# Kernel optimization log

Hardware: AMD Instinct MI355X
Metric: run time of the kernel (lower is better)

Reference implementation:

```python
import jax, jax.numpy as jnp
import numpy as np

NUM_USERS = 100_000
NUM_ITEMS = 400_000
N = NUM_USERS + NUM_ITEMS  # total nodes in bipartite graph
EMB = 64
N_LAYERS = 3
NNZ = 10_000_000


def setup_inputs() -> dict:
    key = jax.random.key(0)
    k1, k2, k3, k4, k5 = jax.random.split(key, 5)
    user_embeddings = jax.random.normal(k1, (NUM_USERS, EMB), dtype=jnp.float32)
    item_embeddings = jax.random.normal(k2, (NUM_ITEMS, EMB), dtype=jnp.float32)
    adj_rows = jax.random.randint(k3, (NNZ,), 0, N, dtype=jnp.int32)
    adj_cols = jax.random.randint(k4, (NNZ,), 0, N, dtype=jnp.int32)
    # symmetric-normalized adjacency values are small positive floats
    adj_vals = jax.random.uniform(k5, (NNZ,), dtype=jnp.float32) * 0.1
    return {
        "user_embeddings": user_embeddings,
        "item_embeddings": item_embeddings,
        "adj_vals": adj_vals,
        "adj_rows": adj_rows,
        "adj_cols": adj_cols,
    }


def _spmm(vals, rows, cols, x):
    # out[r] = sum_{nz : rows[nz]==r} vals[nz] * x[cols[nz]]
    return jax.ops.segment_sum(vals[:, None] * x[cols], rows, num_segments=N)


def reference(user_embeddings, item_embeddings, adj_vals, adj_rows, adj_cols):
    ego = jnp.concatenate([user_embeddings, item_embeddings], axis=0)  # [N, EMB]
    acc = ego
    for _ in range(N_LAYERS):
        ego = _spmm(adj_vals, adj_rows, adj_cols, ego)
        acc = acc + ego
    all_emb = acc / jnp.asarray(N_LAYERS + 1, dtype=ego.dtype)  # layer-mean
    return all_emb[:NUM_USERS], all_emb[NUM_USERS:]
```

## Files before the change

kernel.cpp:

```cpp
#include <hip/hip_runtime.h>


#define NUSERS 100000
#define NNODES 500000
#define EMB 64
#define COLBITS 19
#define CMASK ((1u << COLBITS) - 1u)

#define SBBITS 10
#define SBROWS (1 << SBBITS)
#define SBMASK (SBROWS - 1)
#define NSB ((NNODES + SBROWS - 1) / SBROWS)
#define TILE 7168
#define P2_THREADS 1024
#define P2_K 24
#define P2_CAP (P2_THREADS * P2_K)
#define SLACK_PAIRS 262144

typedef unsigned long long ull;

__device__ __forceinline__ unsigned pk2(float lo, float hi) {
  unsigned a = __float_as_uint(lo);
  unsigned b = __float_as_uint(hi);
  a = (a + 0x7fffu + ((a >> 16) & 1u)) >> 16;
  b = (b + 0x7fffu + ((b >> 16) & 1u)) & 0xffff0000u;
  return (a & 0xffffu) | b;
}
__device__ __forceinline__ float blo(unsigned u) { return __uint_as_float(u << 16); }
__device__ __forceinline__ float bhi(unsigned u) { return __uint_as_float(u & 0xffff0000u); }


__global__ void hist_sb(const int* __restrict__ rows, int nnz,
                        int* __restrict__ counts) {
  __shared__ int h[NSB];
  for (int i = threadIdx.x; i < NSB; i += blockDim.x) h[i] = 0;
  __syncthreads();
  int i = blockIdx.x * blockDim.x + threadIdx.x;
  int stride = gridDim.x * blockDim.x;
  for (; i < nnz; i += stride) atomicAdd(&h[rows[i] >> SBBITS], 1);
  __syncthreads();
  for (int j = threadIdx.x; j < NSB; j += blockDim.x)
    if (h[j]) atomicAdd(&counts[j], h[j]);
}

__global__ void scan_buckets(const int* __restrict__ counts,
                             int* __restrict__ bptr, int* __restrict__ cursor,
                             int n, int nnz) {
  __shared__ int s[512];
  const int t = threadIdx.x;
  const int base = t * 8;
  int e[8];
  int tsum = 0;
#pragma unroll
  for (int j = 0; j < 8; ++j) {
    e[j] = (base + j < n) ? counts[base + j] : 0;
    tsum += e[j];
  }
  s[t] = tsum;
  __syncthreads();
  for (int off = 1; off < 512; off <<= 1) {
    int v = (t >= off) ? s[t - off] : 0;
    __syncthreads();
    s[t] += v;
    __syncthreads();
  }
  int run = s[t] - tsum;
#pragma unroll
  for (int j = 0; j < 8; ++j) {
    if (base + j < n) { bptr[base + j] = run; cursor[base + j] = run; }
    run += e[j];
  }
  if (t == 511) bptr[n] = nnz;
}

__global__ __launch_bounds__(256) void scatter_sb(
    const int* __restrict__ rows, const int* __restrict__ cols,
    const float* __restrict__ vals, int nnz,
    int* __restrict__ cursor, ull* __restrict__ pairs) {
  __shared__ ull stg[TILE];
  __shared__ int cnt[NSB];
  __shared__ int start[NSB];
  __shared__ int sbase[NSB];
  __shared__ int ssc[256];
  const int t = threadIdx.x;
  const int tile0 = blockIdx.x * TILE;
  const int tileN = min(TILE, nnz - tile0);
  if (tileN <= 0) return;

  for (int i = t; i < NSB; i += 256) cnt[i] = 0;
  __syncthreads();

  int rr[TILE / 256];
#pragma unroll
  for (int k = 0; k < TILE / 256; ++k) {
    int idx = tile0 + t + k * 256;
    rr[k] = (idx < nnz) ? rows[idx] : -1;
    if (rr[k] >= 0) atomicAdd(&cnt[rr[k] >> SBBITS], 1);
  }
  __syncthreads();

  {
    const int i0 = 2 * t, i1 = 2 * t + 1;
    int c0 = (i0 < NSB) ? cnt[i0] : 0;
    int c1 = (i1 < NSB) ? cnt[i1] : 0;
    int tsum = c0 + c1;
    ssc[t] = tsum;
    __syncthreads();
    for (int off = 1; off < 256; off <<= 1) {
      int v = (t >= off) ? ssc[t - off] : 0;
      __syncthreads();
      ssc[t] += v;
      __syncthreads();
    }
    int excl = ssc[t] - tsum;
    if (i0 < NSB) start[i0] = excl;
    if (i1 < NSB) start[i1] = excl + c0;
  }
  __syncthreads();

  for (int sb = t; sb < NSB; sb += 256) {
    int c = cnt[sb];
    if (c) sbase[sb] = atomicAdd(&cursor[sb], c);
  }
  __syncthreads();
  for (int i = t; i < NSB; i += 256) cnt[i] = 0;
  __syncthreads();

#pragma unroll
  for (int k = 0; k < TILE / 256; ++k) {
    int idx = tile0 + t + k * 256;
    if (idx < nnz) {
      int r = rr[k];
      int sb = r >> SBBITS;
      unsigned key = ((unsigned)(r & SBMASK) << COLBITS) | (unsigned)cols[idx];
      ull p = ((ull)__float_as_uint(vals[idx]) << 32) | key;
      int j = start[sb] + atomicAdd(&cnt[sb], 1);
      stg[j] = p;
    }
  }
  __syncthreads();

  for (int j = t; j < tileN; j += 256) {
    int lo = 0, hi = NSB - 1;
    while (lo < hi) {
      int mid = (lo + hi + 1) >> 1;
      if (start[mid] <= j) lo = mid; else hi = mid - 1;
    }
    pairs[sbase[lo] + (j - start[lo])] = stg[j];
  }
}

__global__ __launch_bounds__(P2_THREADS) void finalize_sb(
    const int* __restrict__ bptr, ull* __restrict__ pairs,
    int* __restrict__ rs, int* __restrict__ re,
    int* __restrict__ ovf_alloc, int nnz) {
  __shared__ int hist[SBROWS];
  __shared__ int start[SBROWS];
  __shared__ int cur[SBROWS];
  __shared__ int ovf_base;
  const int b = blockIdx.x;
  const int t = threadIdx.x;
  const int s = bptr[b];
  const int n = bptr[b + 1] - s;
  const bool ovf = (n > P2_CAP);

  hist[t] = 0;
  ull* __restrict__ slack = pairs + nnz;
  if (ovf && t == 0) ovf_base = atomicAdd(ovf_alloc, n);
  __syncthreads();

  ull q[P2_K];
  if (!ovf) {
#pragma unroll
    for (int k = 0; k < P2_K; ++k) {
      int idx = t + k * P2_THREADS;
      if (idx < n) {
        q[k] = pairs[s + idx];
        atomicAdd(&hist[(unsigned)q[k] >> COLBITS], 1);
      }
    }
  } else {
    for (int j = t; j < n; j += P2_THREADS) slack[ovf_base + j] = pairs[s + j];
    __syncthreads();
    for (int j = t; j < n; j += P2_THREADS)
      atomicAdd(&hist[(unsigned)slack[ovf_base + j] >> COLBITS], 1);
  }
  __syncthreads();

  start[t] = hist[t];
  __syncthreads();
  for (int off = 1; off < SBROWS; off <<= 1) {
    int v = (t >= off) ? start[t - off] : 0;
    __syncthreads();
    start[t] += v;
    __syncthreads();
  }
  int excl = start[t] - hist[t];
  cur[t] = excl;

  int row = b * SBROWS + t;
  if (row < NNODES) {
    rs[row] = s + excl;
    re[row] = s + excl + hist[t];
  }
  __syncthreads();

  if (!ovf) {
#pragma unroll
    for (int k = 0; k < P2_K; ++k) {
      int idx = t + k * P2_THREADS;
      if (idx < n) {
        unsigned key = (unsigned)q[k];
        int pos = atomicAdd(&cur[key >> COLBITS], 1);
        pairs[s + pos] = ((q[k] >> 32) << 32) | (key & CMASK);
      }
    }
  } else {
    for (int j = t; j < n; j += P2_THREADS) {
      ull p = slack[ovf_base + j];
      unsigned key = (unsigned)p;
      int pos = atomicAdd(&cur[key >> COLBITS], 1);
      pairs[s + pos] = ((p >> 32) << 32) | (key & CMASK);
    }
  }
}

__global__ void conv_e16(const float4* __restrict__ user4,
                         const float4* __restrict__ item4,
                         uint2* __restrict__ E) {
  const int n4 = NNODES * EMB / 4;
  const int u4 = NUSERS * EMB / 4;
  int i = blockIdx.x * blockDim.x + threadIdx.x;
  if (i >= n4) return;
  float4 a = (i < u4) ? user4[i] : item4[i - u4];
  E[i] = make_uint2(pk2(a.x, a.y), pk2(a.z, a.w));
}

template <bool FINAL>
__global__ __launch_bounds__(256) void spmm_bf16(
    const int* __restrict__ rs, const int* __restrict__ re,
    const ull* __restrict__ pq, const ushort* __restrict__ T,
    const float* __restrict__ user_emb, const float* __restrict__ item_emb,
    void* __restrict__ dest, float scale) {
  const int lane = threadIdx.x & 63;
  const int sub  = lane >> 3;
  const int l4   = lane & 7;
  const int wid  = (int)((blockIdx.x * blockDim.x + threadIdx.x) >> 6);
  const int r = wid * 8 + sub;
  if (r >= NNODES) return;
  const int s = rs[r];
  const int e = re[r];
  const uint4* __restrict__ T4 = (const uint4*)T;

  float4 aL0 = make_float4(0.f, 0.f, 0.f, 0.f);
  float4 aH0 = make_float4(0.f, 0.f, 0.f, 0.f);
  float4 aL1 = make_float4(0.f, 0.f, 0.f, 0.f);
  float4 aH1 = make_float4(0.f, 0.f, 0.f, 0.f);

  auto fma8 = [&](float4& L, float4& H, float v, uint4 z) {
    L.x = fmaf(v, blo(z.x), L.x); L.y = fmaf(v, bhi(z.x), L.y);
    L.z = fmaf(v, blo(z.y), L.z); L.w = fmaf(v, bhi(z.y), L.w);
    H.x = fmaf(v, blo(z.z), H.x); H.y = fmaf(v, bhi(z.z), H.y);
    H.z = fmaf(v, blo(z.w), H.z); H.w = fmaf(v, bhi(z.w), H.w);
  };

  int i = s;
  for (; i + 3 < e; i += 4) {
    ull q0 = __builtin_nontemporal_load(&pq[i + 0]);
    ull q1 = __builtin_nontemporal_load(&pq[i + 1]);
    ull q2 = __builtin_nontemporal_load(&pq[i + 2]);
    ull q3 = __builtin_nontemporal_load(&pq[i + 3]);
    uint4 z0 = T4[(size_t)(unsigned)q0 * 8 + l4];
    uint4 z1 = T4[(size_t)(unsigned)q1 * 8 + l4];
    uint4 z2 = T4[(size_t)(unsigned)q2 * 8 + l4];
    uint4 z3 = T4[(size_t)(unsigned)q3 * 8 + l4];
    float v0 = __uint_as_float((unsigned)(q0 >> 32));
    float v1 = __uint_as_float((unsigned)(q1 >> 32));
    float v2 = __uint_as_float((unsigned)(q2 >> 32));
    float v3 = __uint_as_float((unsigned)(q3 >> 32));
    fma8(aL0, aH0, v0, z0);
    fma8(aL1, aH1, v1, z1);
    fma8(aL0, aH0, v2, z2);
    fma8(aL1, aH1, v3, z3);
  }
  for (; i < e; ++i) {
    ull q = __builtin_nontemporal_load(&pq[i]);
    uint4 z = T4[(size_t)(unsigned)q * 8 + l4];
    float v = __uint_as_float((unsigned)(q >> 32));
    fma8(aL0, aH0, v, z);
  }

  float4 aL, aH;
  aL.x = aL0.x + aL1.x; aL.y = aL0.y + aL1.y;
  aL.z = aL0.z + aL1.z; aL.w = aL0.w + aL1.w;
  aH.x = aH0.x + aH1.x; aH.y = aH0.y + aH1.y;
  aH.z = aH0.z + aH1.z; aH.w = aH0.w + aH1.w;

  const ull* e0p = (r < NUSERS)
      ? (const ull*)(user_emb + (size_t)r * EMB)
      : (const ull*)(item_emb + (size_t)(r - NUSERS) * EMB);
  ull eq0 = __builtin_nontemporal_load(&e0p[l4 * 4 + 0]);
  ull eq1 = __builtin_nontemporal_load(&e0p[l4 * 4 + 1]);
  ull eq2 = __builtin_nontemporal_load(&e0p[l4 * 4 + 2]);
  ull eq3 = __builtin_nontemporal_load(&e0p[l4 * 4 + 3]);
  float e0, e1, e2, e3, e4, e5, e6, e7;
  e0 = __uint_as_float((unsigned)eq0); e1 = __uint_as_float((unsigned)(eq0 >> 32));
  e2 = __uint_as_float((unsigned)eq1); e3 = __uint_as_float((unsigned)(eq1 >> 32));
  e4 = __uint_as_float((unsigned)eq2); e5 = __uint_as_float((unsigned)(eq2 >> 32));
  e6 = __uint_as_float((unsigned)eq3); e7 = __uint_as_float((unsigned)(eq3 >> 32));

  if (FINAL) {
    float4 oL, oH;
    oL.x = scale * (e0 + aL.x); oL.y = scale * (e1 + aL.y);
    oL.z = scale * (e2 + aL.z); oL.w = scale * (e3 + aL.w);
    oH.x = scale * (e4 + aH.x); oH.y = scale * (e5 + aH.y);
    oH.z = scale * (e6 + aH.z); oH.w = scale * (e7 + aH.w);
    float4* d4 = (float4*)dest;
    d4[(size_t)r * 16 + l4 * 2 + 0] = oL;
    d4[(size_t)r * 16 + l4 * 2 + 1] = oH;
  } else {
    uint4 ob;
    ob.x = pk2(e0 + aL.x, e1 + aL.y);
    ob.y = pk2(e2 + aL.z, e3 + aL.w);
    ob.z = pk2(e4 + aH.x, e5 + aH.y);
    ob.w = pk2(e6 + aH.z, e7 + aH.w);
    ((uint4*)dest)[(size_t)r * 8 + l4] = ob;
  }
}


__global__ void spmm_atomic(const float* __restrict__ vals,
                            const int* __restrict__ rows,
                            const int* __restrict__ cols,
                            const float* __restrict__ user_emb,
                            const float* __restrict__ item_emb,
                            const float* __restrict__ prev, int nnz,
                            float* __restrict__ y) {
  const int lane = threadIdx.x & 63;
  int wave = (int)((blockIdx.x * blockDim.x + threadIdx.x) >> 6);
  const int nwaves = (int)((gridDim.x * blockDim.x) >> 6);
  for (int nz = wave; nz < nnz; nz += nwaves) {
    float v = vals[nz];
    int r = rows[nz];
    int c = cols[nz];
    float xv = (c < NUSERS) ? user_emb[(size_t)c * EMB + lane]
                            : item_emb[(size_t)(c - NUSERS) * EMB + lane];
    if (prev) xv += prev[(size_t)c * EMB + lane];
    atomicAdd(&y[(size_t)r * EMB + lane], v * xv);
  }
}

__global__ void finalize_kernel(const float4* __restrict__ user4,
                                const float4* __restrict__ item4,
                                float4* __restrict__ X4) {
  const int n4 = NNODES * EMB / 4;
  const int u4 = NUSERS * EMB / 4;
  int i = blockIdx.x * blockDim.x + threadIdx.x;
  if (i >= n4) return;
  float4 a = (i < u4) ? user4[i] : item4[i - u4];
  float4 b = X4[i];
  b.x = 0.25f * (a.x + b.x);
  b.y = 0.25f * (a.y + b.y);
  b.z = 0.25f * (a.z + b.z);
  b.w = 0.25f * (a.w + b.w);
  X4[i] = b;
}


extern "C" void kernel_launch(void* const* d_in, const int* in_sizes, int n_in,
                              void* d_out, int out_size, void* d_ws, size_t ws_size,
                              hipStream_t stream) {
  const float* user_emb = (const float*)d_in[0];
  const float* item_emb = (const float*)d_in[1];
  const float* vals     = (const float*)d_in[2];
  const int*   rows     = (const int*)d_in[3];
  const int*   cols     = (const int*)d_in[4];
  const int nnz = in_sizes[2];
  float* W = (float*)d_out;

  const float4* user4 = (const float4*)user_emb;
  const float4* item4 = (const float4*)item_emb;

  const size_t bfBytes   = (size_t)NNODES * EMB * 2;
  const size_t embBytes  = (size_t)NNODES * EMB * sizeof(float);
  const size_t pairBytes = ((size_t)nnz + SLACK_PAIRS) * sizeof(ull);
  const size_t rsBytes   = ((size_t)NNODES * 4 + 255) & ~(size_t)255;
  const size_t reBytes   = rsBytes;
  const size_t ptrBytes  = ((size_t)(NSB + 1) * 4 + 255) & ~(size_t)255;
  const size_t curBytes  = ((size_t)NSB * 4 + 255) & ~(size_t)255;
  const size_t cntBytes  = ((size_t)NSB * 4 + 255) & ~(size_t)255;
  const size_t ovfBytes  = 256;
  const size_t need = 2 * bfBytes + pairBytes + rsBytes + reBytes + ptrBytes +
                      curBytes + cntBytes + ovfBytes;

  dim3 blk(256);

  if (ws_size < need) {
    float* Y = (float*)d_ws;
    hipMemsetAsync(W, 0, embBytes, stream);
    hipMemsetAsync(Y, 0, embBytes, stream);
    dim3 grid(4096);
    spmm_atomic<<<grid, blk, 0, stream>>>(vals, rows, cols, user_emb, item_emb, nullptr, nnz, W);
    spmm_atomic<<<grid, blk, 0, stream>>>(vals, rows, cols, user_emb, item_emb, W, nnz, Y);
    hipMemsetAsync(W, 0, embBytes, stream);
    spmm_atomic<<<grid, blk, 0, stream>>>(vals, rows, cols, user_emb, item_emb, Y, nnz, W);
    const int n4 = NNODES * EMB / 4;
    finalize_kernel<<<(n4 + 255) / 256, blk, 0, stream>>>(user4, item4, (float4*)W);
    return;
  }

  char* ws = (char*)d_ws;
  ushort* bfA   = (ushort*)ws; ws += bfBytes;
  ushort* bfB   = (ushort*)ws; ws += bfBytes;
  ull*   pairs  = (ull*)ws;    ws += pairBytes;
  int*   rsArr  = (int*)ws;    ws += rsBytes;
  int*   reArr  = (int*)ws;    ws += reBytes;
  int*   bptr   = (int*)ws;    ws += ptrBytes;
  int*   cursor = (int*)ws;    ws += curBytes;
  int*   counts = (int*)ws;    ws += cntBytes;
  int*   ovf    = (int*)ws;

  hipMemsetAsync(counts, 0, (size_t)NSB * 4, stream);
  hipMemsetAsync(ovf, 0, 4, stream);
  hist_sb<<<256, blk, 0, stream>>>(rows, nnz, counts);
  scan_buckets<<<1, 512, 0, stream>>>(counts, bptr, cursor, NSB, nnz);
  const int ntiles = (nnz + TILE - 1) / TILE;
  scatter_sb<<<ntiles, blk, 0, stream>>>(rows, cols, vals, nnz, cursor, pairs);
  finalize_sb<<<NSB, P2_THREADS, 0, stream>>>(bptr, pairs, rsArr, reArr, ovf, nnz);

  const int n4 = NNODES * EMB / 4;
  conv_e16<<<(n4 + 255) / 256, blk, 0, stream>>>(user4, item4, (uint2*)bfA);

  const int sgrid = NNODES / 32;
  spmm_bf16<false><<<sgrid, blk, 0, stream>>>(rsArr, reArr, pairs, bfA,
                                              user_emb, item_emb, bfB, 1.0f);
  spmm_bf16<false><<<sgrid, blk, 0, stream>>>(rsArr, reArr, pairs, bfB,
                                              user_emb, item_emb, bfA, 1.0f);
  spmm_bf16<true ><<<sgrid, blk, 0, stream>>>(rsArr, reArr, pairs, bfA,
                                              user_emb, item_emb, W, 0.25f);
}
```

Measured before the change: 1.325 ms.

## Use per-tile histogram matrix for deterministic scatter bases and LDS-staged finalize

Replaces the global atomic cursor in the bucket scatter with a per-tile histogram pass plus a column-wise prefix scan, so each tile's write base per superblock is precomputed. It also records each staged entry's superblock id in shared memory instead of binary-searching it, halves superblock size to 512 rows with 512-thread finalize blocks, and stages finalize output in LDS so the global writes are coalesced. The cost is an extra pass over rows, a tiles-by-buckets count matrix in workspace, and a serial scan over about 1400 tiles per bucket.

```diff
diff --git a/kernel.cpp b/kernel.cpp
--- a/kernel.cpp
+++ b/kernel.cpp
@@ -7,14 +7,14 @@
 #define COLBITS 19
 #define CMASK ((1u << COLBITS) - 1u)
 
-#define SBBITS 10
+#define SBBITS 9
 #define SBROWS (1 << SBBITS)
 #define SBMASK (SBROWS - 1)
 #define NSB ((NNODES + SBROWS - 1) / SBROWS)
 #define TILE 7168
-#define P2_THREADS 1024
-#define P2_K 24
-#define P2_CAP (P2_THREADS * P2_K)
+#define P2_THREADS 512
+#define P2_CAP 12800
+#define P2_K 25
 #define SLACK_PAIRS 262144
 
 typedef unsigned long long ull;
@@ -73,14 +73,74 @@
   if (t == 511) bptr[n] = nnz;
 }
 
+__global__ __launch_bounds__(256) void tile_hist(const int* __restrict__ rows, int nnz,
+                                                 int* __restrict__ cntmat) {
+  __shared__ int h[NSB];
+  const int t = threadIdx.x;
+  const int tile0 = blockIdx.x * TILE;
+  const int tileN = min(TILE, nnz - tile0);
+  if (tileN <= 0) return;
+  for (int i = t; i < NSB; i += 256) h[i] = 0;
+  __syncthreads();
+  for (int i = t; i < tileN; i += 256) atomicAdd(&h[rows[tile0 + i] >> SBBITS], 1);
+  __syncthreads();
+  int* row = cntmat + (size_t)blockIdx.x * NSB;
+  for (int i = t; i < NSB; i += 256) row[i] = h[i];
+}
+
+__global__ void col_base(int* __restrict__ A, int ntiles,
+                         const int* __restrict__ bptr) {
+  int sb = blockIdx.x * 64 + threadIdx.x;
+  if (sb >= NSB) return;
+  int run = bptr[sb];
+  int t = 0;
+  if (ntiles >= 16) {
+    int b0 = A[(size_t)0 * NSB + sb], b1 = A[(size_t)1 * NSB + sb];
+    int b2 = A[(size_t)2 * NSB + sb], b3 = A[(size_t)3 * NSB + sb];
+    int b4 = A[(size_t)4 * NSB + sb], b5 = A[(size_t)5 * NSB + sb];
+    int b6 = A[(size_t)6 * NSB + sb], b7 = A[(size_t)7 * NSB + sb];
+    for (; t + 16 <= ntiles; t += 8) {
+      int n0 = A[(size_t)(t + 8) * NSB + sb],  n1 = A[(size_t)(t + 9) * NSB + sb];
+      int n2 = A[(size_t)(t + 10) * NSB + sb], n3 = A[(size_t)(t + 11) * NSB + sb];
+      int n4 = A[(size_t)(t + 12) * NSB + sb], n5 = A[(size_t)(t + 13) * NSB + sb];
+      int n6 = A[(size_t)(t + 14) * NSB + sb], n7 = A[(size_t)(t + 15) * NSB + sb];
+      A[(size_t)(t + 0) * NSB + sb] = run; run += b0;
+      A[(size_t)(t + 1) * NSB + sb] = run; run += b1;
+      A[(size_t)(t + 2) * NSB + sb] = run; run += b2;
+      A[(size_t)(t + 3) * NSB + sb] = run; run += b3;
+      A[(size_t)(t + 4) * NSB + sb] = run; run += b4;
+      A[(size_t)(t + 5) * NSB + sb] = run; run += b5;
+      A[(size_t)(t + 6) * NSB + sb] = run; run += b6;
+      A[(size_t)(t + 7) * NSB + sb] = run; run += b7;
+      b0 = n0; b1 = n1; b2 = n2; b3 = n3;
+      b4 = n4; b5 = n5; b6 = n6; b7 = n7;
+    }
+    A[(size_t)(t + 0) * NSB + sb] = run; run += b0;
+    A[(size_t)(t + 1) * NSB + sb] = run; run += b1;
+    A[(size_t)(t + 2) * NSB + sb] = run; run += b2;
+    A[(size_t)(t + 3) * NSB + sb] = run; run += b3;
+    A[(size_t)(t + 4) * NSB + sb] = run; run += b4;
+    A[(size_t)(t + 5) * NSB + sb] = run; run += b5;
+    A[(size_t)(t + 6) * NSB + sb] = run; run += b6;
+    A[(size_t)(t + 7) * NSB + sb] = run; run += b7;
+    t += 8;
+  }
+  for (; t < ntiles; ++t) {
+    size_t i = (size_t)t * NSB + sb;
+    int c = A[i];
+    A[i] = run;
+    run += c;
+  }
+}
+
 __global__ __launch_bounds__(256) void scatter_sb(
     const int* __restrict__ rows, const int* __restrict__ cols,
     const float* __restrict__ vals, int nnz,
-    int* __restrict__ cursor, ull* __restrict__ pairs) {
+    const int* __restrict__ basemat, ull* __restrict__ pairs) {
   __shared__ ull stg[TILE];
+  __shared__ ushort sbid[TILE];
   __shared__ int cnt[NSB];
   __shared__ int start[NSB];
-  __shared__ int sbase[NSB];
   __shared__ int ssc[256];
   const int t = threadIdx.x;
   const int tile0 = blockIdx.x * TILE;
@@ -100,10 +160,14 @@
   __syncthreads();
 
   {
-    const int i0 = 2 * t, i1 = 2 * t + 1;
-    int c0 = (i0 < NSB) ? cnt[i0] : 0;
-    int c1 = (i1 < NSB) ? cnt[i1] : 0;
-    int tsum = c0 + c1;
+    int c[4];
+    int tsum = 0;
+#pragma unroll
+    for (int j = 0; j < 4; ++j) {
+      int i = t * 4 + j;
+      c[j] = (i < NSB) ? cnt[i] : 0;
+      tsum += c[j];
+    }
     ssc[t] = tsum;
     __syncthreads();
     for (int off = 1; off < 256; off <<= 1) {
@@ -112,15 +176,13 @@
       ssc[t] += v;
       __syncthreads();
     }
-    int excl = ssc[t] - tsum;
-    if (i0 < NSB) start[i0] = excl;
-    if (i1 < NSB) start[i1] = excl + c0;
-  }
-  __syncthreads();
-
-  for (int sb = t; sb < NSB; sb += 256) {
-    int c = cnt[sb];
-    if (c) sbase[sb] = atomicAdd(&cursor[sb], c);
+    int run = ssc[t] - tsum;
+#pragma unroll
+    for (int j = 0; j < 4; ++j) {
+      int i = t * 4 + j;
+      if (i < NSB) start[i] = run;
+      run += c[j];
+    }
   }
   __syncthreads();
   for (int i = t; i < NSB; i += 256) cnt[i] = 0;
@@ -136,17 +198,15 @@
       ull p = ((ull)__float_as_uint(vals[idx]) << 32) | key;
       int j = start[sb] + atomicAdd(&cnt[sb], 1);
       stg[j] = p;
-    }
-  }
-  __syncthreads();
-
+      sbid[j] = (ushort)sb;
+    }
+  }
+  __syncthreads();
+
+  const int* __restrict__ baserow = basemat + (size_t)blockIdx.x * NSB;
   for (int j = t; j < tileN; j += 256) {
-    int lo = 0, hi = NSB - 1;
-    while (lo < hi) {
-      int mid = (lo + hi + 1) >> 1;
-      if (start[mid] <= j) lo = mid; else hi = mid - 1;
-    }
-    pairs[sbase[lo] + (j - start[lo])] = stg[j];
+    int sb = sbid[j];
+    pairs[baserow[sb] + (j - start[sb])] = stg[j];
   }
 }
 
@@ -157,6 +217,7 @@
   __shared__ int hist[SBROWS];
   __shared__ int start[SBROWS];
   __shared__ int cur[SBROWS];
+  __shared__ ull out[P2_CAP];
   __shared__ int ovf_base;
   const int b = blockIdx.x;
   const int t = threadIdx.x;
@@ -212,9 +273,11 @@
       if (idx < n) {
         unsigned key = (unsigned)q[k];
         int pos = atomicAdd(&cur[key >> COLBITS], 1);
-        pairs[s + pos] = ((q[k] >> 32) << 32) | (key & CMASK);
+        out[pos] = ((q[k] >> 32) << 32) | (key & CMASK);
       }
     }
+    __syncthreads();
+    for (int j = t; j < n; j += P2_THREADS) pairs[s + j] = out[j];
   } else {
     for (int j = t; j < n; j += P2_THREADS) {
       ull p = slack[ovf_base + j];
@@ -381,6 +444,8 @@
   const float4* user4 = (const float4*)user_emb;
   const float4* item4 = (const float4*)item_emb;
 
+  const int ntiles = (nnz + TILE - 1) / TILE;
+
   const size_t bfBytes   = (size_t)NNODES * EMB * 2;
   const size_t embBytes  = (size_t)NNODES * EMB * sizeof(float);
   const size_t pairBytes = ((size_t)nnz + SLACK_PAIRS) * sizeof(ull);
@@ -389,9 +454,10 @@
   const size_t ptrBytes  = ((size_t)(NSB + 1) * 4 + 255) & ~(size_t)255;
   const size_t curBytes  = ((size_t)NSB * 4 + 255) & ~(size_t)255;
   const size_t cntBytes  = ((size_t)NSB * 4 + 255) & ~(size_t)255;
+  const size_t matBytes  = (((size_t)ntiles * NSB * 4) + 255) & ~(size_t)255;
   const size_t ovfBytes  = 256;
   const size_t need = 2 * bfBytes + pairBytes + rsBytes + reBytes + ptrBytes +
-                      curBytes + cntBytes + ovfBytes;
+                      curBytes + cntBytes + matBytes + ovfBytes;
 
   dim3 blk(256);
 
@@ -418,14 +484,16 @@
   int*   bptr   = (int*)ws;    ws += ptrBytes;
   int*   cursor = (int*)ws;    ws += curBytes;
   int*   counts = (int*)ws;    ws += cntBytes;
+  int*   cntmat = (int*)ws;    ws += matBytes;
   int*   ovf    = (int*)ws;
 
   hipMemsetAsync(counts, 0, (size_t)NSB * 4, stream);
   hipMemsetAsync(ovf, 0, 4, stream);
   hist_sb<<<256, blk, 0, stream>>>(rows, nnz, counts);
   scan_buckets<<<1, 512, 0, stream>>>(counts, bptr, cursor, NSB, nnz);
-  const int ntiles = (nnz + TILE - 1) / TILE;
-  scatter_sb<<<ntiles, blk, 0, stream>>>(rows, cols, vals, nnz, cursor, pairs);
+  tile_hist<<<ntiles, blk, 0, stream>>>(rows, nnz, cntmat);
+  col_base<<<(NSB + 63) / 64, 64, 0, stream>>>(cntmat, ntiles, bptr);
+  scatter_sb<<<ntiles, blk, 0, stream>>>(rows, cols, vals, nnz, cntmat, pairs);
   finalize_sb<<<NSB, P2_THREADS, 0, stream>>>(bptr, pairs, rsArr, reArr, ovf, nnz);
 
   const int n4 = NNODES * EMB / 4;
```

Measured after the change: 1.334 ms. About the same (+0.7%).
